# Kernel optimization log

Hardware: AMD Instinct MI355X
Metric: run time of the kernel (lower is better)

The kernel has to match this reference:

```python
import jax, jax.numpy as jnp
import numpy as np

B, S, H = 2, 2048, 4096
NH, NKV, HD = 32, 8, 128
ROPE_THETA = 10000.0


def _rope_tables(seq_len, head_dim, theta):
    inv_freq = 1.0 / (theta ** (jnp.arange(0, head_dim, 2, dtype=jnp.float32) / head_dim))
    t = jnp.arange(seq_len, dtype=jnp.float32)
    freqs = jnp.outer(t, inv_freq)            # [S, HD/2]
    emb = jnp.concatenate([freqs, freqs], axis=-1)  # [S, HD]
    return jnp.cos(emb), jnp.sin(emb)


def _rotate_half(x):
    x1, x2 = jnp.split(x, 2, axis=-1)
    return jnp.concatenate([-x2, x1], axis=-1)


def setup_inputs() -> dict:
    key = jax.random.key(0)
    ks = jax.random.split(key, 5)
    hidden_states = jax.random.normal(ks[0], (B, S, H), dtype=jnp.float32)
    # causal additive mask [B,1,S,S]
    neg = jnp.finfo(jnp.float32).min
    causal = jnp.where(jnp.tril(jnp.ones((S, S), dtype=bool)), 0.0, neg)
    attention_mask = jnp.broadcast_to(causal[None, None], (B, 1, S, S)).astype(jnp.float32)
    position_ids = jnp.broadcast_to(jnp.arange(S, dtype=jnp.int64)[None], (B, S))
    scale = 0.02
    Wq = jax.random.normal(ks[1], (H, H), dtype=jnp.float32) * scale
    Wk = jax.random.normal(ks[2], (NKV * HD, H), dtype=jnp.float32) * scale
    Wv = jax.random.normal(ks[3], (NKV * HD, H), dtype=jnp.float32) * scale
    Wo = jax.random.normal(ks[4], (H, H), dtype=jnp.float32) * scale
    return {"hidden_states": hidden_states, "attention_mask": attention_mask,
            "position_ids": position_ids, "Wq": Wq, "Wk": Wk, "Wv": Wv, "Wo": Wo}


def reference(hidden_states, attention_mask, position_ids, Wq, Wk, Wv, Wo):
    bsz, q_len, _ = hidden_states.shape
    # projections (nn.Linear: x @ W.T)
    q = (hidden_states @ Wq.T).reshape(bsz, q_len, NH, HD).transpose(0, 2, 1, 3)    # [B,NH,S,HD]
    k = (hidden_states @ Wk.T).reshape(bsz, q_len, NKV, HD).transpose(0, 2, 1, 3)   # [B,NKV,S,HD]
    v = (hidden_states @ Wv.T).reshape(bsz, q_len, NKV, HD).transpose(0, 2, 1, 3)
    # RoPE
    cos, sin = _rope_tables(q_len, HD, ROPE_THETA)
    cos = cos[position_ids][:, None]   # [B,1,S,HD]
    sin = sin[position_ids][:, None]
    q = q * cos + _rotate_half(q) * sin
    k = k * cos + _rotate_half(k) * sin
    # repeat_kv (GQA): [B,NKV,S,HD] -> [B,NH,S,HD]
    n_rep = NH // NKV
    k = jnp.repeat(k, n_rep, axis=1)
    v = jnp.repeat(v, n_rep, axis=1)
    # attention
    attn = jnp.einsum('bhqd,bhkd->bhqk', q, k) / jnp.sqrt(jnp.float32(HD))
    attn = attn + attention_mask
    attn = jax.nn.softmax(attn.astype(jnp.float32), axis=-1).astype(q.dtype)
    out = jnp.einsum('bhqk,bhkd->bhqd', attn, v)           # [B,NH,S,HD]
    out = out.transpose(0, 2, 1, 3).reshape(bsz, q_len, NH * HD)
    return out @ Wo.T
```

## Files before the change

### kernel.cpp

```cpp
#include <hip/hip_runtime.h>
#include <hip/hip_bf16.h>


typedef __bf16 bf16;
typedef __bf16 bf16x8 __attribute__((ext_vector_type(8)));
typedef float f32x4 __attribute__((ext_vector_type(4)));

#define UNROLL _Pragma("unroll")

__device__ __forceinline__ void async16(const bf16* g, bf16* l) {
  __builtin_amdgcn_global_load_lds(
      (const __attribute__((address_space(1))) void*)g,
      (__attribute__((address_space(3))) void*)l,
      16, 0, 0);
}

#define BARR { __builtin_amdgcn_s_barrier(); }
#define VMCNT(n) { asm volatile("s_waitcnt vmcnt(" #n ")" ::: "memory"); }

__global__ void k_cvt(const float* __restrict__ s, bf16* __restrict__ d, int n8) {
  int i = blockIdx.x * 256 + threadIdx.x;
  if (i >= n8) return;
  const float4* sp = (const float4*)s + (size_t)i * 2;
  float4 a = sp[0], b = sp[1];
  bf16x8 o = { (bf16)a.x, (bf16)a.y, (bf16)a.z, (bf16)a.w,
               (bf16)b.x, (bf16)b.y, (bf16)b.z, (bf16)b.w };
  *(bf16x8*)(d + (size_t)i * 8) = o;
}

__global__ void k_cvtw3(const float* __restrict__ Wq, const float* __restrict__ Wk,
                        const float* __restrict__ Wv, bf16* __restrict__ Wqkv) {
  int u = blockIdx.x * 256 + threadIdx.x;
  const float* sp;
  bf16* dp;
  size_t off;
  if (u < 2097152) { sp = Wq; dp = Wqkv; off = u; }
  else if (u < 2621440) { sp = Wk; dp = Wqkv + 16777216u; off = u - 2097152; }
  else { sp = Wv; dp = Wqkv + 20971520u; off = u - 2621440; }
  const float4* s4 = (const float4*)sp + off * 2;
  float4 a = s4[0], b = s4[1];
  bf16x8 o = { (bf16)a.x, (bf16)a.y, (bf16)a.z, (bf16)a.w,
               (bf16)b.x, (bf16)b.y, (bf16)b.z, (bf16)b.w };
  *(bf16x8*)(dp + off * 8) = o;
}

template <typename OutT>
__global__ __launch_bounds__(512, 2) void k_gemmCS(
    const bf16* __restrict__ A, const bf16* __restrict__ Bw,
    OutT* __restrict__ C, int K, int N, int nbx) {
  __shared__ __align__(16) bf16 lds[2][4][8192];
  const int tid = threadIdx.x;
  const int lane = tid & 63;
  const int w = tid >> 6;
  const int wm = w >> 2, wn = w & 3;
  const int l16 = lane & 15, lh = lane >> 4;

  const int cpx = gridDim.x >> 3;
  const int swz = (blockIdx.x & 7) * cpx + (blockIdx.x >> 3);
  const int by = swz / nbx, bx = swz % nbx;
  const size_t m0 = (size_t)by * 256, n0 = (size_t)bx * 256;

  const int row0 = tid >> 2;
  const int cOff = ((tid & 3) ^ ((row0 >> 1) & 3)) * 8;
  const bf16* pA0 = A + (m0 + row0) * K + cOff;
  const bf16* pA1 = pA0 + (size_t)128 * K;
  const bf16* pB0 = Bw + (n0 + row0) * K + cOff;
  const bf16* pB1 = pB0 + (size_t)128 * K;

#define SA(s, h, t)                                        \
  { const int kk = (t) * 64 + (h) * 32;                    \
    async16(pA0 + kk, &lds[s][h][0] + tid * 8);            \
    async16(pA1 + kk, &lds[s][h][0] + 4096 + tid * 8); }
#define SB(s, h, t)                                        \
  { const int kk = (t) * 64 + (h) * 32;                    \
    async16(pB0 + kk, &lds[s][2 + (h)][0] + tid * 8);      \
    async16(pB1 + kk, &lds[s][2 + (h)][0] + 4096 + tid * 8); }

#define RDA(s, u, mh)                                                 \
  UNROLL for (int x = 0; x < 4; ++x) {                                \
    int p = (wm * 128 + (mh) * 64 + x * 16 + l16) * 64 + lh * 16;     \
    p ^= ((p >> 7) & 3) << 4;                                         \
    Ar[x] = *(const bf16x8*)((const char*)&lds[s][u][0] + p);         \
  }
#define RDB(s, u)                                                     \
  UNROLL for (int y = 0; y < 4; ++y) {                                \
    int p = (wn * 64 + y * 16 + l16) * 64 + lh * 16;                  \
    p ^= ((p >> 7) & 3) << 4;                                         \
    Br[y] = *(const bf16x8*)((const char*)&lds[s][u][0] + p);         \
  }
#define MF(mh)                                                        \
  { __builtin_amdgcn_s_setprio(1);                                    \
    UNROLL for (int x = 0; x < 4; ++x)                                \
      UNROLL for (int y = 0; y < 4; ++y)                              \
        acc[(mh) * 4 + x][y] = __builtin_amdgcn_mfma_f32_16x16x32_bf16( \
            Ar[x], Br[y], acc[(mh) * 4 + x][y], 0, 0, 0);             \
    __builtin_amdgcn_s_setprio(0); }

  f32x4 acc[8][4] = {};
  const int NITER = K >> 7;

  SA(0, 0, 0); SB(0, 0, 0); SA(0, 1, 0); SB(0, 1, 0); SA(1, 0, 1); SB(1, 0, 1);
  VMCNT(8);

#define ITER_BODY(i, LAST)                                                  \
  { const int t0 = 2 * (i), t1 = t0 + 1;                                    \
    bf16x8 Ar[4], Br[4];                                                    \
    BARR; RDA(0, 0, 0); RDB(0, 2); SA(1, 1, t1); MF(0);                     \
    BARR; RDA(0, 0, 1); SB(1, 1, t1); MF(1); VMCNT(8);                      \
    BARR; RDA(0, 1, 0); RDB(0, 3); if (!(LAST)) SA(0, 0, t0 + 2); MF(0);    \
    BARR; RDA(0, 1, 1); if (!(LAST)) SB(0, 0, t0 + 2); MF(1);               \
    if (LAST) { VMCNT(4); } else { VMCNT(8); }                              \
    BARR; RDA(1, 0, 0); RDB(1, 2); if (!(LAST)) SA(0, 1, t0 + 2); MF(0);    \
    BARR; RDA(1, 0, 1); if (!(LAST)) SB(0, 1, t0 + 2); MF(1);               \
    if (LAST) { VMCNT(0); } else { VMCNT(8); }                              \
    BARR; RDA(1, 1, 0); RDB(1, 3); if (!(LAST)) SA(1, 0, t1 + 2); MF(0);    \
    BARR; RDA(1, 1, 1); if (!(LAST)) SB(1, 0, t1 + 2); MF(1);               \
    if (!(LAST)) VMCNT(8); }

  for (int i = 0; i < NITER - 1; ++i) ITER_BODY(i, 0);
  ITER_BODY(NITER - 1, 1);

  UNROLL for (int mi = 0; mi < 8; ++mi) {
    size_t row = m0 + wm * 128 + mi * 16 + lh * 4;
    UNROLL for (int ni = 0; ni < 4; ++ni) {
      size_t col = n0 + wn * 64 + ni * 16 + l16;
      UNROLL for (int j = 0; j < 4; ++j)
        C[(row + j) * N + col] = (OutT)acc[mi][ni][j];
    }
  }
#undef SA
#undef SB
#undef RDA
#undef RDB
#undef MF
#undef ITER_BODY
}

__global__ void k_rope(const bf16* __restrict__ QKV, bf16* __restrict__ Qr,
                       bf16* __restrict__ Kr) {
  int gid = blockIdx.x * 256 + threadIdx.x;
  int seg = gid & 7;
  int rest = gid >> 3;
  int slot = rest % 40;
  int tok = rest / 40;
  int s = tok & 2047;
  int b = tok >> 11;
  const bf16* src = QKV + (size_t)tok * 6144 + slot * 128 + seg * 8;
  bf16x8 a = *(const bf16x8*)src;
  bf16x8 c = *(const bf16x8*)(src + 64);
  bf16x8 o1v, o2v;
  const float scale = (slot < 32) ? 0.08838834764831845f : 1.0f;
  UNROLL for (int j = 0; j < 8; ++j) {
    int p = seg * 8 + j;
    float f = exp2f((float)p * (-13.287712379549449f / 64.0f));
    float sn, cn;
    sincosf((float)s * f, &sn, &cn);
    float x1 = (float)a[j], x2 = (float)c[j];
    o1v[j] = (bf16)((x1 * cn - x2 * sn) * scale);
    o2v[j] = (bf16)((x2 * cn + x1 * sn) * scale);
  }
  bf16* dst;
  if (slot < 32) {
    dst = Qr + (((size_t)b * 32 + slot) * 2048 + s) * 128 + seg * 8;
  } else {
    dst = Kr + (((size_t)b * 8 + (slot - 32)) * 2048 + s) * 128 + seg * 8;
  }
  *(bf16x8*)dst = o1v;
  *(bf16x8*)(dst + 64) = o2v;
}

__global__ void k_vtrans(const bf16* __restrict__ QKV, bf16* __restrict__ Vtg) {
  __shared__ __align__(16) bf16 T[64 * 64];
  const int tid = threadIdx.x;
  const int dt = blockIdx.x & 1;
  const int st = (blockIdx.x >> 1) & 31;
  const int hh = blockIdx.x >> 6;
  const int hkv = hh & 7, b = hh >> 3;
  const int s0 = st * 64, d0 = dt * 64;
  const bf16* src = QKV + (size_t)(b * 2048 + s0) * 6144 + 5120 + hkv * 128 + d0;
  UNROLL for (int k = 0; k < 2; ++k) {
    int cc = tid * 2 + k;
    int r = cc >> 3, c8 = cc & 7;
    bf16x8 v = *(const bf16x8*)(src + (size_t)r * 6144 + c8 * 8);
    int byte = (r * 128 + c8 * 16) ^ ((r & 7) << 4);
    *(bf16x8*)((char*)T + byte) = v;
  }
  __syncthreads();
  bf16* dst = Vtg + ((size_t)(b * 8 + hkv) * 128 + d0) * 2048 + s0;
  UNROLL for (int k = 0; k < 2; ++k) {
    int cc = tid * 2 + k;
    int d = cc >> 3, s8 = cc & 7;
    bf16x8 v;
    UNROLL for (int j = 0; j < 8; ++j) {
      int s = s8 * 8 + j;
      int byte = (s * 128 + d * 2) ^ ((s & 7) << 4);
      v[j] = *(const bf16*)((const char*)T + byte);
    }
    *(bf16x8*)(dst + (size_t)d * 2048 + s8 * 8) = v;
  }
}

__global__ __launch_bounds__(256, 2) void k_flash(
    const bf16* __restrict__ Qr, const bf16* __restrict__ Kr,
    const bf16* __restrict__ Vtg, bf16* __restrict__ Out) {
  __shared__ __align__(16) bf16 Kl[2][64 * 128];
  __shared__ __align__(16) bf16 Vl[2][128 * 64];
  __shared__ __align__(16) bf16 Pl[4][32 * 64];
  const int tid = threadIdx.x;
  const int lane = tid & 63;
  const int w = tid >> 6;
  const int l16 = lane & 15, lh = lane >> 4;
  const int pid = blockIdx.x & 7;
  const int hl = blockIdx.x >> 3;
  const int h = hl & 31, b = hl >> 5;
  const int hkv = h >> 2;
  const bf16* Kbase = Kr + ((size_t)(b * 8 + hkv)) * 2048 * 128;
  const bf16* Vbase = Vtg + ((size_t)(b * 8 + hkv)) * 128 * 2048;
  bf16* P = &Pl[w][0];

  int kOff[4], vOff[4], ldsOff[4];
  UNROLL for (int i = 0; i < 4; ++i) {
    int c = (w * 4 + i) * 64 + lane;
    ldsOff[i] = c * 8;
    int r = c >> 4, p = c & 15;
    kOff[i] = r * 128 + (p ^ (r & 7)) * 8;
    int r2 = c >> 3, p2 = c & 7;
    vOff[i] = r2 * 2048 + (p2 ^ (r2 & 7)) * 8;
  }

  for (int qi = 0; qi < 2; ++qi) {
    const int q = qi ? (15 - pid) : pid;
    const int q0 = q * 128;
    const int nt = 2 * q + 2;

    bf16x8 qf[2][4];
    UNROLL for (int m = 0; m < 2; ++m) {
      const bf16* qb = Qr + (((size_t)(b * 32 + h)) * 2048 + q0 + w * 32 + m * 16 + l16) * 128 + lh * 8;
      UNROLL for (int kc = 0; kc < 4; ++kc) qf[m][kc] = *(const bf16x8*)(qb + kc * 32);
    }
    f32x4 acc[2][8] = {};
    float mrow[2][4] = {{-1e30f, -1e30f, -1e30f, -1e30f}, {-1e30f, -1e30f, -1e30f, -1e30f}};
    float lrow[2][4] = {};

    UNROLL for (int i = 0; i < 4; ++i) {
      async16(Kbase + kOff[i], &Kl[0][0] + ldsOff[i]);
      async16(Vbase + vOff[i], &Vl[0][0] + ldsOff[i]);
    }
    __syncthreads();

    for (int t = 0; t < nt; ++t) {
      const int cur = t & 1;
      if (t + 1 < nt) {
        const int nb = t + 1;
        UNROLL for (int i = 0; i < 4; ++i) {
          async16(Kbase + (size_t)nb * 8192 + kOff[i], &Kl[cur ^ 1][0] + ldsOff[i]);
          async16(Vbase + (size_t)nb * 64 + vOff[i], &Vl[cur ^ 1][0] + ldsOff[i]);
        }
      }
      f32x4 sf[2][4] = {};
      UNROLL for (int ni = 0; ni < 4; ++ni) {
        int row = ni * 16 + l16;
        bf16x8 kf[4];
        UNROLL for (int kc = 0; kc < 4; ++kc) {
          int byte = (row * 256 + kc * 64 + lh * 16) ^ ((row & 7) << 4);
          kf[kc] = *(const bf16x8*)((const char*)&Kl[cur][0] + byte);
        }
        UNROLL for (int m = 0; m < 2; ++m)
          UNROLL for (int kc = 0; kc < 4; ++kc)
            sf[m][ni] = __builtin_amdgcn_mfma_f32_16x16x32_bf16(qf[m][kc], kf[kc], sf[m][ni], 0, 0, 0);
      }
      if (t >= 2 * q) {
        UNROLL for (int m = 0; m < 2; ++m)
          UNROLL for (int ni = 0; ni < 4; ++ni) {
            int key = t * 64 + ni * 16 + l16;
            UNROLL for (int j = 0; j < 4; ++j) {
              int rowg = q0 + w * 32 + m * 16 + lh * 4 + j;
              if (key > rowg) sf[m][ni][j] = -1e30f;
            }
          }
      }
      float corr[2][4];
      UNROLL for (int m = 0; m < 2; ++m)
        UNROLL for (int j = 0; j < 4; ++j) {
          float mx = fmaxf(fmaxf(sf[m][0][j], sf[m][1][j]), fmaxf(sf[m][2][j], sf[m][3][j]));
          mx = fmaxf(mx, __shfl_xor(mx, 1));
          mx = fmaxf(mx, __shfl_xor(mx, 2));
          mx = fmaxf(mx, __shfl_xor(mx, 4));
          mx = fmaxf(mx, __shfl_xor(mx, 8));
          float mn = fmaxf(mrow[m][j], mx);
          corr[m][j] = __expf(mrow[m][j] - mn);
          mrow[m][j] = mn;
          float rs = 0.f;
          UNROLL for (int ni = 0; ni < 4; ++ni) {
            float pv = __expf(sf[m][ni][j] - mn);
            sf[m][ni][j] = pv;
            rs += pv;
          }
          rs += __shfl_xor(rs, 1);
          rs += __shfl_xor(rs, 2);
          rs += __shfl_xor(rs, 4);
          rs += __shfl_xor(rs, 8);
          lrow[m][j] = lrow[m][j] * corr[m][j] + rs;
        }
      UNROLL for (int m = 0; m < 2; ++m)
        UNROLL for (int di = 0; di < 8; ++di)
          UNROLL for (int j = 0; j < 4; ++j) acc[m][di][j] *= corr[m][j];
      UNROLL for (int m = 0; m < 2; ++m)
        UNROLL for (int ni = 0; ni < 4; ++ni)
          UNROLL for (int j = 0; j < 4; ++j) {
            int row = m * 16 + lh * 4 + j;
            int byte = (row * 128 + ni * 32 + l16 * 2) ^ ((row & 7) << 4);
            *(bf16*)((char*)P + byte) = (bf16)sf[m][ni][j];
          }
      UNROLL for (int kc = 0; kc < 2; ++kc) {
        bf16x8 pa[2];
        UNROLL for (int m = 0; m < 2; ++m) {
          int row = m * 16 + l16;
          int byte = (row * 128 + kc * 64 + lh * 16) ^ ((row & 7) << 4);
          pa[m] = *(const bf16x8*)((const char*)P + byte);
        }
        UNROLL for (int di = 0; di < 8; ++di) {
          int d = di * 16 + l16;
          int byte = (d * 128 + kc * 64 + lh * 16) ^ ((d & 7) << 4);
          bf16x8 vb = *(const bf16x8*)((const char*)&Vl[cur][0] + byte);
          UNROLL for (int m = 0; m < 2; ++m)
            acc[m][di] = __builtin_amdgcn_mfma_f32_16x16x32_bf16(pa[m], vb, acc[m][di], 0, 0, 0);
        }
      }
      __syncthreads();
    }

    UNROLL for (int m = 0; m < 2; ++m)
      UNROLL for (int j = 0; j < 4; ++j) {
        float inv = 1.0f / lrow[m][j];
        int rowg = q0 + w * 32 + m * 16 + lh * 4 + j;
        bf16* ob = Out + ((size_t)(b * 2048) + rowg) * 4096 + h * 128 + l16;
        UNROLL for (int di = 0; di < 8; ++di)
          ob[di * 16] = (bf16)(acc[m][di][j] * inv);
      }
  }
}

extern "C" void kernel_launch(void* const* d_in, const int* in_sizes, int n_in,
                              void* d_out, int out_size, void* d_ws, size_t ws_size,
                              hipStream_t stream) {
  const float* hidden = (const float*)d_in[0];
  const float* Wq = (const float*)d_in[3];
  const float* Wk = (const float*)d_in[4];
  const float* Wv = (const float*)d_in[5];
  const float* Wo = (const float*)d_in[6];
  float* out = (float*)d_out;

  char* ws = (char*)d_ws;
  if (ws_size < 184549376u) return;
  bf16* Xb = (bf16*)(ws);
  bf16* Wqkv = (bf16*)(ws + 33554432u);
  bf16* QKV = (bf16*)(ws + 83886080u);
  bf16* Qr = (bf16*)(ws + 134217728u);
  bf16* Kr = (bf16*)(ws + 167772160u);
  bf16* Vtg = (bf16*)(ws + 176160768u);
  bf16* AttnO = Xb;
  bf16* Wob = Wqkv;

  k_cvt<<<8192, 256, 0, stream>>>(hidden, Xb, 2097152);
  k_cvtw3<<<12288, 256, 0, stream>>>(Wq, Wk, Wv, Wqkv);
  k_gemmCS<bf16><<<384, 512, 0, stream>>>(Xb, Wqkv, QKV, 4096, 6144, 24);
  k_rope<<<5120, 256, 0, stream>>>(QKV, Qr, Kr);
  k_vtrans<<<1024, 256, 0, stream>>>(QKV, Vtg);
  k_cvt<<<8192, 256, 0, stream>>>(Wo, Wob, 2097152);
  k_flash<<<512, 256, 0, stream>>>(Qr, Kr, Vtg, AttnO);
  k_gemmCS<float><<<256, 512, 0, stream>>>(AttnO, Wob, out, 4096, 4096, 16);
}
```

Baseline: 574.4 us.

## Replace 256x256 GEMM with 128x128-tile register double-buffered pipelined GEMM

Replaces the 512-thread 256x256-tile GEMM with a 256-thread 128x128-tile kernel. It keeps two register fragment sets, so LDS reads for the next half-k-step overlap the MFMAs of the current one, with one barrier per half step instead of eight per iteration. The smaller tiles mean more blocks (1536 and 1024 instead of 384 and 256), which should fill the CUs better and give finer load balance. The cost is lower per-block data reuse and more global and L2 traffic for operand tiles.

```diff
diff --git a/kernel.cpp b/kernel.cpp
--- a/kernel.cpp
+++ b/kernel.cpp
@@ -45,95 +45,94 @@
 }
 
 template <typename OutT>
-__global__ __launch_bounds__(512, 2) void k_gemmCS(
+__global__ __launch_bounds__(256, 2) void k_gemmPL(
     const bf16* __restrict__ A, const bf16* __restrict__ Bw,
     OutT* __restrict__ C, int K, int N, int nbx) {
-  __shared__ __align__(16) bf16 lds[2][4][8192];
+  __shared__ __align__(16) bf16 lds[2][4][4096];
   const int tid = threadIdx.x;
   const int lane = tid & 63;
   const int w = tid >> 6;
-  const int wm = w >> 2, wn = w & 3;
+  const int wm = w >> 1, wn = w & 1;
   const int l16 = lane & 15, lh = lane >> 4;
 
   const int cpx = gridDim.x >> 3;
   const int swz = (blockIdx.x & 7) * cpx + (blockIdx.x >> 3);
   const int by = swz / nbx, bx = swz % nbx;
-  const size_t m0 = (size_t)by * 256, n0 = (size_t)bx * 256;
+  const size_t m0 = (size_t)by * 128, n0 = (size_t)bx * 128;
 
   const int row0 = tid >> 2;
-  const int cOff = ((tid & 3) ^ ((row0 >> 1) & 3)) * 8;
-  const bf16* pA0 = A + (m0 + row0) * K + cOff;
-  const bf16* pA1 = pA0 + (size_t)128 * K;
-  const bf16* pB0 = Bw + (n0 + row0) * K + cOff;
-  const bf16* pB1 = pB0 + (size_t)128 * K;
-
-#define SA(s, h, t)                                        \
-  { const int kk = (t) * 64 + (h) * 32;                    \
-    async16(pA0 + kk, &lds[s][h][0] + tid * 8);            \
-    async16(pA1 + kk, &lds[s][h][0] + 4096 + tid * 8); }
-#define SB(s, h, t)                                        \
-  { const int kk = (t) * 64 + (h) * 32;                    \
-    async16(pB0 + kk, &lds[s][2 + (h)][0] + tid * 8);      \
-    async16(pB1 + kk, &lds[s][2 + (h)][0] + 4096 + tid * 8); }
-
-#define RDA(s, u, mh)                                                 \
+  const int cOff = ((tid & 3) ^ ((tid >> 3) & 3)) * 8;
+  const bf16* pAa = A + (m0 + row0) * K + cOff;
+  const bf16* pAb = pAa + (size_t)64 * K;
+  const bf16* pBa = Bw + (n0 + row0) * K + cOff;
+  const bf16* pBb = pBa + (size_t)64 * K;
+
+#define SAU(s, h, t)                                      \
+  { const int kk = (t) * 64 + (h) * 32;                   \
+    async16(pAa + kk, &lds[s][h][0] + tid * 8);           \
+    async16(pAb + kk, &lds[s][h][0] + 2048 + tid * 8); }
+#define SBU(s, h, t)                                      \
+  { const int kk = (t) * 64 + (h) * 32;                   \
+    async16(pBa + kk, &lds[s][2 + (h)][0] + tid * 8);     \
+    async16(pBb + kk, &lds[s][2 + (h)][0] + 2048 + tid * 8); }
+
+#define RD_A(dst, s, h)                                               \
   UNROLL for (int x = 0; x < 4; ++x) {                                \
-    int p = (wm * 128 + (mh) * 64 + x * 16 + l16) * 64 + lh * 16;     \
+    int p = (wm * 64 + x * 16 + l16) * 64 + lh * 16;                  \
     p ^= ((p >> 7) & 3) << 4;                                         \
-    Ar[x] = *(const bf16x8*)((const char*)&lds[s][u][0] + p);         \
-  }
-#define RDB(s, u)                                                     \
+    dst[x] = *(const bf16x8*)((const char*)&lds[s][h][0] + p);        \
+  }
+#define RD_B(dst, s, h)                                               \
   UNROLL for (int y = 0; y < 4; ++y) {                                \
     int p = (wn * 64 + y * 16 + l16) * 64 + lh * 16;                  \
     p ^= ((p >> 7) & 3) << 4;                                         \
-    Br[y] = *(const bf16x8*)((const char*)&lds[s][u][0] + p);         \
-  }
-#define MF(mh)                                                        \
+    dst[y] = *(const bf16x8*)((const char*)&lds[s][2 + (h)][0] + p);  \
+  }
+#define MFM(Asrc, Bsrc)                                               \
   { __builtin_amdgcn_s_setprio(1);                                    \
     UNROLL for (int x = 0; x < 4; ++x)                                \
       UNROLL for (int y = 0; y < 4; ++y)                              \
-        acc[(mh) * 4 + x][y] = __builtin_amdgcn_mfma_f32_16x16x32_bf16( \
-            Ar[x], Br[y], acc[(mh) * 4 + x][y], 0, 0, 0);             \
+        acc[x][y] = __builtin_amdgcn_mfma_f32_16x16x32_bf16(          \
+            Asrc[x], Bsrc[y], acc[x][y], 0, 0, 0);                    \
     __builtin_amdgcn_s_setprio(0); }
 
-  f32x4 acc[8][4] = {};
-  const int NITER = K >> 7;
-
-  SA(0, 0, 0); SB(0, 0, 0); SA(0, 1, 0); SB(0, 1, 0); SA(1, 0, 1); SB(1, 0, 1);
-  VMCNT(8);
-
-#define ITER_BODY(i, LAST)                                                  \
-  { const int t0 = 2 * (i), t1 = t0 + 1;                                    \
-    bf16x8 Ar[4], Br[4];                                                    \
-    BARR; RDA(0, 0, 0); RDB(0, 2); SA(1, 1, t1); MF(0);                     \
-    BARR; RDA(0, 0, 1); SB(1, 1, t1); MF(1); VMCNT(8);                      \
-    BARR; RDA(0, 1, 0); RDB(0, 3); if (!(LAST)) SA(0, 0, t0 + 2); MF(0);    \
-    BARR; RDA(0, 1, 1); if (!(LAST)) SB(0, 0, t0 + 2); MF(1);               \
-    if (LAST) { VMCNT(4); } else { VMCNT(8); }                              \
-    BARR; RDA(1, 0, 0); RDB(1, 2); if (!(LAST)) SA(0, 1, t0 + 2); MF(0);    \
-    BARR; RDA(1, 0, 1); if (!(LAST)) SB(0, 1, t0 + 2); MF(1);               \
-    if (LAST) { VMCNT(0); } else { VMCNT(8); }                              \
-    BARR; RDA(1, 1, 0); RDB(1, 3); if (!(LAST)) SA(1, 0, t1 + 2); MF(0);    \
-    BARR; RDA(1, 1, 1); if (!(LAST)) SB(1, 0, t1 + 2); MF(1);               \
-    if (!(LAST)) VMCNT(8); }
-
-  for (int i = 0; i < NITER - 1; ++i) ITER_BODY(i, 0);
-  ITER_BODY(NITER - 1, 1);
-
-  UNROLL for (int mi = 0; mi < 8; ++mi) {
-    size_t row = m0 + wm * 128 + mi * 16 + lh * 4;
+  f32x4 acc[4][4] = {};
+  const int NT = K >> 6;
+  bf16x8 Ar0[4], Br0[4], Ar1[4], Br1[4];
+
+  SAU(0, 0, 0); SBU(0, 0, 0); SAU(0, 1, 0); SBU(0, 1, 0);
+  SAU(1, 0, 1); SBU(1, 0, 1);
+  VMCNT(4);
+  BARR;
+  RD_A(Ar1, 0, 0); RD_B(Br1, 0, 0);
+
+  for (int t = 0; t < NT; ++t) {
+    const int s = t & 1;
+    BARR;
+    RD_A(Ar0, s, 1); RD_B(Br0, s, 1);
+    if (t + 1 < NT) { SAU(s ^ 1, 1, t + 1); SBU(s ^ 1, 1, t + 1); }
+    MFM(Ar1, Br1);
+    if (t + 1 < NT) VMCNT(4);
+    BARR;
+    if (t + 1 < NT) { RD_A(Ar1, s ^ 1, 0); RD_B(Br1, s ^ 1, 0); }
+    if (t + 2 < NT) { SAU(s, 0, t + 2); SBU(s, 0, t + 2); }
+    MFM(Ar0, Br0);
+    if (t + 2 < NT) { VMCNT(4); } else if (t + 2 == NT) { VMCNT(0); }
+  }
+
+  UNROLL for (int mi = 0; mi < 4; ++mi) {
+    size_t row = m0 + wm * 64 + mi * 16 + lh * 4;
     UNROLL for (int ni = 0; ni < 4; ++ni) {
       size_t col = n0 + wn * 64 + ni * 16 + l16;
       UNROLL for (int j = 0; j < 4; ++j)
         C[(row + j) * N + col] = (OutT)acc[mi][ni][j];
     }
   }
-#undef SA
-#undef SB
-#undef RDA
-#undef RDB
-#undef MF
-#undef ITER_BODY
+#undef SAU
+#undef SBU
+#undef RD_A
+#undef RD_B
+#undef MFM
 }
 
 __global__ void k_rope(const bf16* __restrict__ QKV, bf16* __restrict__ Qr,
@@ -364,10 +363,10 @@
 
   k_cvt<<<8192, 256, 0, stream>>>(hidden, Xb, 2097152);
   k_cvtw3<<<12288, 256, 0, stream>>>(Wq, Wk, Wv, Wqkv);
-  k_gemmCS<bf16><<<384, 512, 0, stream>>>(Xb, Wqkv, QKV, 4096, 6144, 24);
+  k_gemmPL<bf16><<<1536, 256, 0, stream>>>(Xb, Wqkv, QKV, 4096, 6144, 48);
   k_rope<<<5120, 256, 0, stream>>>(QKV, Qr, Kr);
   k_vtrans<<<1024, 256, 0, stream>>>(QKV, Vtg);
   k_cvt<<<8192, 256, 0, stream>>>(Wo, Wob, 2097152);
   k_flash<<<512, 256, 0, stream>>>(Qr, Kr, Vtg, AttnO);
-  k_gemmCS<float><<<256, 512, 0, stream>>>(AttnO, Wob, out, 4096, 4096, 16);
-}
+  k_gemmPL<float><<<1024, 256, 0, stream>>>(AttnO, Wob, out, 4096, 4096, 32);
+}
```

Result: slower. 668.9 us (+16.5%).

## Split QKV GEMM into Q GEMM and split-K KV GEMM with reduction

Applied to the files above, without the earlier changes.

The fused QKV projection is replaced by a Q-only GEMM and a K/V GEMM that splits the K dimension in two. Each half is written as a bf16 partial, and a new reduction kernel sums the halves into the QKV buffer. The goal is to even out work across CUs, since the 384-tile grid mapped unevenly onto the device. In exchange it adds extra launches and a partial-sum round trip through memory, and rounding the partials to bf16 costs some precision.

```diff
diff --git a/kernel.cpp b/kernel.cpp
--- a/kernel.cpp
+++ b/kernel.cpp
@@ -44,10 +44,10 @@
   *(bf16x8*)(dp + off * 8) = o;
 }
 
-template <typename OutT>
+template <typename OutT, int SPLIT>
 __global__ __launch_bounds__(512, 2) void k_gemmCS(
     const bf16* __restrict__ A, const bf16* __restrict__ Bw,
-    OutT* __restrict__ C, int K, int N, int nbx) {
+    OutT* __restrict__ C, int lda, int Kloop, int ldc, int nbx, size_t csplit) {
   __shared__ __align__(16) bf16 lds[2][4][8192];
   const int tid = threadIdx.x;
   const int lane = tid & 63;
@@ -57,15 +57,27 @@
 
   const int cpx = gridDim.x >> 3;
   const int swz = (blockIdx.x & 7) * cpx + (blockIdx.x >> 3);
-  const int by = swz / nbx, bx = swz % nbx;
+  int by, bx;
+  if (SPLIT) {
+    const int kh = swz >> 7;
+    const int t = swz & 127;
+    by = t >> 3;
+    bx = t & 7;
+    A += (size_t)kh * 2048;
+    Bw += (size_t)kh * 2048;
+    C += (size_t)kh * csplit;
+  } else {
+    by = swz / nbx;
+    bx = swz % nbx;
+  }
   const size_t m0 = (size_t)by * 256, n0 = (size_t)bx * 256;
 
   const int row0 = tid >> 2;
   const int cOff = ((tid & 3) ^ ((row0 >> 1) & 3)) * 8;
-  const bf16* pA0 = A + (m0 + row0) * K + cOff;
-  const bf16* pA1 = pA0 + (size_t)128 * K;
-  const bf16* pB0 = Bw + (n0 + row0) * K + cOff;
-  const bf16* pB1 = pB0 + (size_t)128 * K;
+  const bf16* pA0 = A + (m0 + row0) * lda + cOff;
+  const bf16* pA1 = pA0 + (size_t)128 * lda;
+  const bf16* pB0 = Bw + (n0 + row0) * lda + cOff;
+  const bf16* pB1 = pB0 + (size_t)128 * lda;
 
 #define SA(s, h, t)                                        \
   { const int kk = (t) * 64 + (h) * 32;                    \
@@ -97,7 +109,7 @@
     __builtin_amdgcn_s_setprio(0); }
 
   f32x4 acc[8][4] = {};
-  const int NITER = K >> 7;
+  const int NITER = Kloop >> 7;
 
   SA(0, 0, 0); SB(0, 0, 0); SA(0, 1, 0); SB(0, 1, 0); SA(1, 0, 1); SB(1, 0, 1);
   VMCNT(8);
@@ -125,7 +137,7 @@
     UNROLL for (int ni = 0; ni < 4; ++ni) {
       size_t col = n0 + wn * 64 + ni * 16 + l16;
       UNROLL for (int j = 0; j < 4; ++j)
-        C[(row + j) * N + col] = (OutT)acc[mi][ni][j];
+        C[(row + j) * ldc + col] = (OutT)acc[mi][ni][j];
     }
   }
 #undef SA
@@ -134,6 +146,18 @@
 #undef RDB
 #undef MF
 #undef ITER_BODY
+}
+
+__global__ void k_redsum(const bf16* __restrict__ s, bf16* __restrict__ QKV) {
+  int i = blockIdx.x * 256 + threadIdx.x;
+  int e = i * 8;
+  int tok = e >> 11;
+  int c = e & 2047;
+  bf16x8 a = *(const bf16x8*)(s + e);
+  bf16x8 b = *(const bf16x8*)(s + 8388608 + e);
+  bf16x8 o;
+  UNROLL for (int j = 0; j < 8; ++j) o[j] = (bf16)((float)a[j] + (float)b[j]);
+  *(bf16x8*)(QKV + (size_t)tok * 6144 + 4096 + c) = o;
 }
 
 __global__ void k_rope(const bf16* __restrict__ QKV, bf16* __restrict__ Qr,
@@ -361,13 +385,17 @@
   bf16* Vtg = (bf16*)(ws + 176160768u);
   bf16* AttnO = Xb;
   bf16* Wob = Wqkv;
+  bf16* Spart = Qr;
 
   k_cvt<<<8192, 256, 0, stream>>>(hidden, Xb, 2097152);
   k_cvtw3<<<12288, 256, 0, stream>>>(Wq, Wk, Wv, Wqkv);
-  k_gemmCS<bf16><<<384, 512, 0, stream>>>(Xb, Wqkv, QKV, 4096, 6144, 24);
+  k_gemmCS<bf16, 0><<<256, 512, 0, stream>>>(Xb, Wqkv, QKV, 4096, 4096, 6144, 16, 0);
+  k_gemmCS<bf16, 1><<<256, 512, 0, stream>>>(
+      Xb, Wqkv + (size_t)4096 * 4096, Spart, 4096, 2048, 2048, 8, 8388608u);
+  k_redsum<<<4096, 256, 0, stream>>>(Spart, QKV);
   k_rope<<<5120, 256, 0, stream>>>(QKV, Qr, Kr);
   k_vtrans<<<1024, 256, 0, stream>>>(QKV, Vtg);
   k_cvt<<<8192, 256, 0, stream>>>(Wo, Wob, 2097152);
   k_flash<<<512, 256, 0, stream>>>(Qr, Kr, Vtg, AttnO);
-  k_gemmCS<float><<<256, 512, 0, stream>>>(AttnO, Wob, out, 4096, 4096, 16);
-}
+  k_gemmCS<float, 0><<<256, 512, 0, stream>>>(AttnO, Wob, out, 4096, 4096, 4096, 16, 0);
+}
```

New measurement: 556.5 us. -3.1%, faster.
